# Kernel optimization log

Hardware: AMD Instinct MI355X
Metric: run time of the kernel (lower is better)

## Reference

```python
import jax, jax.numpy as jnp
import numpy as np

WIN = (2, 7, 7)
SHIFT = (1, 3, 3)
HEADS = 4
DIM = 128
MLP_HID = 512
N = WIN[0] * WIN[1] * WIN[2]  # 98
EPS = 1e-5


def _rel_pos_index():
    d = np.arange(WIN[0]); h = np.arange(WIN[1]); w = np.arange(WIN[2])
    coords = np.stack(np.meshgrid(d, h, w, indexing='ij'))  # (3, Wd, Wh, Ww)
    flat = coords.reshape(3, -1)  # (3, N)
    rel = flat[:, :, None] - flat[:, None, :]  # (3, N, N)
    rel = rel.transpose(1, 2, 0).astype(np.int64)  # (N, N, 3)
    rel[..., 0] += WIN[0] - 1
    rel[..., 1] += WIN[1] - 1
    rel[..., 2] += WIN[2] - 1
    rel[..., 0] *= (2 * WIN[1] - 1) * (2 * WIN[2] - 1)
    rel[..., 1] *= (2 * WIN[2] - 1)
    return rel.sum(-1)  # (N, N)


def setup_inputs() -> dict:
    key = jax.random.key(0)
    ks = jax.random.split(key, 8)
    B, D, H, W, C = 4, 8, 56, 56, DIM
    tbl_size = (2 * WIN[0] - 1) * (2 * WIN[1] - 1) * (2 * WIN[2] - 1)  # 507
    s = 0.02
    return {
        'x': jax.random.normal(ks[0], (B, D, H, W, C), jnp.float32),
        'rel_idx': jnp.asarray(_rel_pos_index(), jnp.int32),
        'rpb_table': s * jax.random.normal(ks[1], (tbl_size, HEADS), jnp.float32),
        'qkv_w': s * jax.random.normal(ks[2], (C, 3 * C), jnp.float32),
        'qkv_b': jnp.zeros((3 * C,), jnp.float32),
        'proj_w': s * jax.random.normal(ks[3], (C, C), jnp.float32),
        'proj_b': jnp.zeros((C,), jnp.float32),
        'ln1_g': jnp.ones((C,), jnp.float32),
        'ln1_b': jnp.zeros((C,), jnp.float32),
        'ln2_g': jnp.ones((C,), jnp.float32),
        'ln2_b': jnp.zeros((C,), jnp.float32),
        'mlp_w1': s * jax.random.normal(ks[4], (C, MLP_HID), jnp.float32),
        'mlp_b1': jnp.zeros((MLP_HID,), jnp.float32),
        'mlp_w2': s * jax.random.normal(ks[5], (MLP_HID, C), jnp.float32),
        'mlp_b2': jnp.zeros((C,), jnp.float32),
    }


def _layernorm(x, g, b):
    mu = jnp.mean(x, -1, keepdims=True)
    var = jnp.var(x, -1, keepdims=True)
    return (x - mu) * jax.lax.rsqrt(var + EPS) * g + b


def _window_partition(x):
    B, Dp, Hp, Wp, C = x.shape
    x = x.reshape(B, Dp // WIN[0], WIN[0], Hp // WIN[1], WIN[1], Wp // WIN[2], WIN[2], C)
    x = x.transpose(0, 1, 3, 5, 2, 4, 6, 7)
    return x.reshape(-1, N, C)


def _window_reverse(win, B, Dp, Hp, Wp):
    C = win.shape[-1]
    x = win.reshape(B, Dp // WIN[0], Hp // WIN[1], Wp // WIN[2], WIN[0], WIN[1], WIN[2], C)
    x = x.transpose(0, 1, 4, 2, 5, 3, 6, 7)
    return x.reshape(B, Dp, Hp, Wp, C)


def _block(x, rel_idx, rpb_table, qkv_w, qkv_b, proj_w, proj_b,
           ln1_g, ln1_b, ln2_g, ln2_b, mlp_w1, mlp_b1, mlp_w2, mlp_b2):
    B, D, H, W, C = x.shape
    shortcut = x
    x = _layernorm(x, ln1_g, ln1_b)
    pad_d = (-D) % WIN[0]; pad_h = (-H) % WIN[1]; pad_w = (-W) % WIN[2]
    x = jnp.pad(x, ((0, 0), (0, pad_d), (0, pad_h), (0, pad_w), (0, 0)))
    _, Dp, Hp, Wp, _ = x.shape
    x = jnp.roll(x, (-SHIFT[0], -SHIFT[1], -SHIFT[2]), axis=(1, 2, 3))
    xw = _window_partition(x)  # (B_, N, C)
    B_ = xw.shape[0]
    hd = C // HEADS
    qkv = (xw @ qkv_w + qkv_b).reshape(B_, N, 3, HEADS, hd).transpose(2, 0, 3, 1, 4)
    q, k, v = qkv[0], qkv[1], qkv[2]  # (B_, h, N, hd)
    q = q * (hd ** -0.5)
    attn = jnp.einsum('bhnd,bhmd->bhnm', q, k)
    bias = rpb_table[rel_idx.reshape(-1)].reshape(N, N, HEADS).transpose(2, 0, 1)
    attn = attn + bias[None]
    # NOTE: the original module calls attn with mask=None even when shifted.
    attn = jax.nn.softmax(attn, axis=-1)
    out = jnp.einsum('bhnm,bhmd->bhnd', attn, v).transpose(0, 2, 1, 3).reshape(B_, N, C)
    out = out @ proj_w + proj_b
    x = _window_reverse(out, B, Dp, Hp, Wp)
    x = jnp.roll(x, (SHIFT[0], SHIFT[1], SHIFT[2]), axis=(1, 2, 3))
    x = x[:, :D, :H, :W, :]
    x = shortcut + x
    h1 = _layernorm(x, ln2_g, ln2_b)
    h1 = jax.nn.gelu(h1 @ mlp_w1 + mlp_b1, approximate=False)
    return x + (h1 @ mlp_w2 + mlp_b2)


def reference(x, rel_idx, rpb_table, qkv_w, qkv_b, proj_w, proj_b,
              ln1_g, ln1_b, ln2_g, ln2_b, mlp_w1, mlp_b1, mlp_w2, mlp_b2):
    return _block(x, rel_idx, rpb_table, qkv_w, qkv_b, proj_w, proj_b,
                  ln1_g, ln1_b, ln2_g, ln2_b, mlp_w1, mlp_b1, mlp_w2, mlp_b2)
```

## Files before the change

### kernel.cpp

```cpp
#include <hip/hip_runtime.h>
#include <hip/hip_bf16.h>
#include <cstdint>

#define NWIN   1024
#define NTOK   98
#define BIAS_N 9604

typedef __attribute__((ext_vector_type(8))) short bf16x8;
typedef __attribute__((ext_vector_type(4))) float f32x4;

__device__ __forceinline__ float b2f(unsigned short u) {
  union { uint32_t i; float f; } v; v.i = ((uint32_t)u) << 16; return v.f;
}
__device__ __forceinline__ float b2f_lo(uint32_t u) {
  union { uint32_t i; float f; } v; v.i = u << 16; return v.f;
}
__device__ __forceinline__ float b2f_hi(uint32_t u) {
  union { uint32_t i; float f; } v; v.i = u & 0xffff0000u; return v.f;
}
__device__ __forceinline__ unsigned short f2b(float f) {
  union { float f; uint32_t i; } v; v.f = f;
  uint32_t r = v.i + 0x7fffu + ((v.i >> 16) & 1u);
  return (unsigned short)(r >> 16);
}
__device__ __forceinline__ float ldf(const void* p, size_t i, int f32) {
  return f32 ? ((const float*)p)[i] : b2f(((const unsigned short*)p)[i]);
}
__device__ __forceinline__ float2 ldf2(const void* p, size_t i, int f32) {
  if (f32) { const float* q = (const float*)p + i; return make_float2(q[0], q[1]); }
  uint32_t u = *(const uint32_t*)((const unsigned short*)p + i);
  return make_float2(b2f_lo(u), b2f_hi(u));
}
__device__ __forceinline__ float gelu_f(float x) {
  float a = fabsf(x) * 0.70710678118654752f;
  float t = __builtin_amdgcn_rcpf(1.0f + 0.3275911f * a);
  float p = ((((1.061405429f * t - 1.453152027f) * t + 1.421413741f) * t
              - 0.284496736f) * t + 0.254829592f) * t;
  float erfp = 1.0f - p * __expf(-a * a);
  return 0.5f * x * (1.0f + copysignf(erfp, x));
}

#define QG_OFF   0
#define KG_OFF   25690112
#define VGT_OFF  51380224
#define ZPAD_OFF 80740352
#define BIAS_OFF 80748544
#define WQ_OFF   80902208
#define WP_OFF   81000512
#define W1_OFF   81033280
#define W2_OFF   81164352
#define PAR_OFF  81295424
#define FLAG_OFF 81302080
#define LNG_OFF  81302144
#define P_LN1G 0
#define P_LN1B 128
#define P_LN2G 256
#define P_LN2B 384
#define P_QKVB 512
#define P_PROJB 896
#define P_B1  1024
#define P_B2  1536

__global__ __launch_bounds__(256) void detect_kernel(const uint32_t* __restrict__ xw,
                                                     int* __restrict__ flag) {
  __shared__ int cnt;
  if (threadIdx.x == 0) cnt = 0;
  __syncthreads();
  uint32_t w = xw[threadIdx.x];
  int e = (w >> 23) & 0xFF;
  if (e >= 112 && e <= 134) atomicAdd(&cnt, 1);
  __syncthreads();
  if (threadIdx.x == 0) *flag = (cnt >= 128) ? 1 : 0;
}

__global__ __launch_bounds__(256) void prep_kernel(
    const void* __restrict__ qkvw, const void* __restrict__ projw,
    const void* __restrict__ w1, const void* __restrict__ w2,
    const void* __restrict__ ln1g, const void* __restrict__ ln1b,
    const void* __restrict__ ln2g, const void* __restrict__ ln2b,
    const void* __restrict__ qkvb, const void* __restrict__ projb,
    const void* __restrict__ b1, const void* __restrict__ b2,
    const int* __restrict__ flag,
    unsigned short* __restrict__ wq_t, unsigned short* __restrict__ wp_t,
    unsigned short* __restrict__ w1_t, unsigned short* __restrict__ w2_t,
    float* __restrict__ par, unsigned short* __restrict__ zpad) {
  const int f32 = *flag;
  int idx = blockIdx.x * 256 + threadIdx.x;
  if (idx < 49152) {
    int n = idx >> 7, k = idx & 127;
    wq_t[idx] = f2b(ldf(qkvw, (size_t)k * 384 + n, f32));
  } else if ((idx -= 49152) < 16384) {
    int n = idx >> 7, k = idx & 127;
    wp_t[idx] = f2b(ldf(projw, (size_t)k * 128 + n, f32));
  } else if ((idx -= 16384) < 65536) {
    int n = idx >> 7, k = idx & 127;
    w1_t[idx] = f2b(ldf(w1, (size_t)k * 512 + n, f32));
  } else if ((idx -= 65536) < 65536) {
    int n = idx >> 9, k = idx & 511;
    w2_t[idx] = f2b(ldf(w2, (size_t)k * 128 + n, f32));
  } else if ((idx -= 65536) < 1664) {
    float v;
    if      (idx < 128)  v = ldf(ln1g, idx, f32);
    else if (idx < 256)  v = ldf(ln1b, idx - 128, f32);
    else if (idx < 384)  v = ldf(ln2g, idx - 256, f32);
    else if (idx < 512)  v = ldf(ln2b, idx - 384, f32);
    else if (idx < 896)  v = ldf(qkvb, idx - 512, f32);
    else if (idx < 1024) v = ldf(projb, idx - 896, f32);
    else if (idx < 1536) v = ldf(b1, idx - 1024, f32);
    else                 v = ldf(b2, idx - 1536, f32);
    par[idx] = v;
  } else if ((idx -= 1664) < 4096) {
    zpad[idx] = 0;
  }
}

__global__ __launch_bounds__(256) void bias_kernel(const int* __restrict__ rel_idx,
                                                   const void* __restrict__ tbl,
                                                   const int* __restrict__ flag,
                                                   float* __restrict__ bias) {
  const int f32 = *flag;
  int i = blockIdx.x * 256 + threadIdx.x;
  if (i >= 4 * BIAS_N) return;
  int h = i / BIAS_N, ij = i % BIAS_N;
  bias[i] = ldf(tbl, (size_t)rel_idx[ij] * 4 + h, f32);
}

__global__ __launch_bounds__(256, 2) void attn_fused_kernel(
    const void* __restrict__ x, const int* __restrict__ flag,
    const unsigned short* __restrict__ wq_t, const float* __restrict__ bias,
    const unsigned short* __restrict__ wp_t, const float* __restrict__ par,
    unsigned short* __restrict__ vgt, unsigned short* __restrict__ lng,
    void* __restrict__ out) {
  __shared__ __align__(16) unsigned short smem[38416];
  const int f32 = *flag;
  const int tid = threadIdx.x, wave = tid >> 6, lane = tid & 63;
  const int quad = lane >> 4, lcol = lane & 15;
  const int win = blockIdx.x, h = wave;
  const int bb = win >> 8, rW = win & 255;
  const int wd = rW >> 6, r2 = rW & 63, wh = r2 >> 3, ww = r2 & 7;

  unsigned short* lnx = smem;
  unsigned short* qs  = smem + 13328;
  unsigned short* ks  = smem + 25872;

  for (int t = wave; t < NTOK; t += 4) {
    int td = t / 49, r3 = t % 49, th = r3 / 7, tw = r3 % 7;
    int sd = (wd * 2 + td + 1) & 7;
    int sh = (wh * 7 + th + 3) % 56;
    int sw = (ww * 7 + tw + 3) % 56;
    size_t src = ((((size_t)bb * 8 + sd) * 56 + sh) * 56 + sw) * 128;
    int c0 = lane * 2;
    float2 f = ldf2(x, src + c0, f32);
    float s = f.x + f.y, ss = f.x * f.x + f.y * f.y;
#pragma unroll
    for (int off = 32; off >= 1; off >>= 1) { s += __shfl_xor(s, off); ss += __shfl_xor(ss, off); }
    float mu = s * (1.0f / 128.0f);
    float var = ss * (1.0f / 128.0f) - mu * mu;
    float rs = rsqrtf(var + 1e-5f);
    float y0 = (f.x - mu) * rs * par[P_LN1G + c0] + par[P_LN1B + c0];
    float y1 = (f.y - mu) * rs * par[P_LN1G + c0 + 1] + par[P_LN1B + c0 + 1];
    *(uint32_t*)(lnx + t * 136 + c0) = (uint32_t)f2b(y0) | ((uint32_t)f2b(y1) << 16);
  }
  __syncthreads();

  for (int p = 0; p < 6; ++p) {
    const int n = p * 64 + wave * 16 + lcol;
    bf16x8 bfr[4];
#pragma unroll
    for (int ks4 = 0; ks4 < 4; ++ks4)
      bfr[ks4] = *(const bf16x8*)(wq_t + (size_t)n * 128 + ks4 * 32 + quad * 8);
    const int region = p >> 1;
    const int head = (p & 1) * 2 + (wave >> 1);
    const int d = (wave & 1) * 16 + lcol;
    const float bc = par[P_QKVB + n];
    if (region < 2) {
      unsigned short* dstl = (region == 0 ? qs : ks) + head * 3136 + d;
      const float scale = region == 0 ? 0.17677669529663687f : 1.0f;
      for (int mt = 0; mt < 7; ++mt) {
        f32x4 acc = (f32x4){0.f, 0.f, 0.f, 0.f};
#pragma unroll
        for (int ks4 = 0; ks4 < 4; ++ks4) {
          bf16x8 a = *(const bf16x8*)(lnx + min(mt * 16 + lcol, NTOK - 1) * 136 +
                                      ks4 * 32 + quad * 8);
          acc = __builtin_amdgcn_mfma_f32_16x16x32_bf16(a, bfr[ks4], acc, 0, 0, 0);
        }
#pragma unroll
        for (int rr = 0; rr < 4; ++rr) {
          int m = mt * 16 + quad * 4 + rr;
          if (m < NTOK) dstl[m * 32] = f2b((acc[rr] + bc) * scale);
        }
      }
    } else {
      unsigned short* dstv = vgt + (((size_t)win * 4 + head) * 32 + d) * 112;
      for (int mt = 0; mt < 7; ++mt) {
        f32x4 acc = (f32x4){0.f, 0.f, 0.f, 0.f};
#pragma unroll
        for (int ks4 = 0; ks4 < 4; ++ks4) {
          bf16x8 a = *(const bf16x8*)(lnx + min(mt * 16 + lcol, NTOK - 1) * 136 +
                                      ks4 * 32 + quad * 8);
          acc = __builtin_amdgcn_mfma_f32_16x16x32_bf16(a, bfr[ks4], acc, 0, 0, 0);
        }
        ushort4 w;
        int m0 = mt * 16 + quad * 4;
        w.x = (m0 + 0 < NTOK) ? f2b(acc[0] + bc) : (unsigned short)0;
        w.y = (m0 + 1 < NTOK) ? f2b(acc[1] + bc) : (unsigned short)0;
        w.z = (m0 + 2 < NTOK) ? f2b(acc[2] + bc) : (unsigned short)0;
        w.w = (m0 + 3 < NTOK) ? f2b(acc[3] + bc) : (unsigned short)0;
        *(ushort4*)(dstv + m0) = w;
      }
    }
  }
  __syncthreads();

  const unsigned short* vbase = vgt + (((size_t)win * 4 + h) * 32) * 112;
  unsigned short* plh = smem + h * 2112;

  bf16x8 aq[7], bk[7];
#pragma unroll
  for (int t = 0; t < 7; ++t) {
    int row = min(t * 16 + lcol, NTOK - 1);
    aq[t] = *(const bf16x8*)(qs + h * 3136 + row * 32 + quad * 8);
    bk[t] = *(const bf16x8*)(ks + h * 3136 + row * 32 + quad * 8);
  }
  for (int idx = lane; idx < 16 * 16; idx += 64) {
    int rr = idx >> 4, c = 112 + (idx & 15);
    plh[rr * 132 + c] = 0;
  }

  const float* bh = bias + h * BIAS_N;
  f32x4 o[7][2];
  for (int mt = 0; mt < 7; ++mt) {
    f32x4 s[7];
#pragma unroll
    for (int nt = 0; nt < 7; ++nt)
      s[nt] = __builtin_amdgcn_mfma_f32_16x16x32_bf16(aq[mt], bk[nt],
                                                      (f32x4){0.f, 0.f, 0.f, 0.f}, 0, 0, 0);
    const int ib = mt * 16 + quad * 4;
#pragma unroll
    for (int nt = 0; nt < 7; ++nt) {
      int j = nt * 16 + lcol;
      bool jv = j < NTOK;
#pragma unroll
      for (int r = 0; r < 4; ++r) {
        int ic = min(ib + r, NTOK - 1);
        s[nt][r] = jv ? (s[nt][r] + bh[ic * NTOK + j]) : -3.0e38f;
      }
    }
    float mx[4], sum[4], inv[4];
#pragma unroll
    for (int r = 0; r < 4; ++r) {
      float m = s[0][r];
#pragma unroll
      for (int nt = 1; nt < 7; ++nt) m = fmaxf(m, s[nt][r]);
      mx[r] = m;
    }
#pragma unroll
    for (int off = 1; off < 16; off <<= 1)
#pragma unroll
      for (int r = 0; r < 4; ++r) mx[r] = fmaxf(mx[r], __shfl_xor(mx[r], off));
#pragma unroll
    for (int r = 0; r < 4; ++r) sum[r] = 0.f;
#pragma unroll
    for (int nt = 0; nt < 7; ++nt)
#pragma unroll
      for (int r = 0; r < 4; ++r) {
        float e = __expf(s[nt][r] - mx[r]);
        s[nt][r] = e; sum[r] += e;
      }
#pragma unroll
    for (int off = 1; off < 16; off <<= 1)
#pragma unroll
      for (int r = 0; r < 4; ++r) sum[r] += __shfl_xor(sum[r], off);
#pragma unroll
    for (int r = 0; r < 4; ++r) inv[r] = 1.0f / sum[r];
#pragma unroll
    for (int nt = 0; nt < 7; ++nt)
#pragma unroll
      for (int r = 0; r < 4; ++r)
        plh[(quad * 4 + r) * 132 + nt * 16 + lcol] = f2b(s[nt][r] * inv[r]);
#pragma unroll
    for (int n2 = 0; n2 < 2; ++n2) {
      f32x4 acc = (f32x4){0.f, 0.f, 0.f, 0.f};
#pragma unroll
      for (int kp = 0; kp < 4; ++kp) {
        bf16x8 a = *(const bf16x8*)(plh + lcol * 132 + kp * 32 + quad * 8);
        bf16x8 b = *(const bf16x8*)(vbase + (size_t)(n2 * 16 + lcol) * 112 +
                                    kp * 32 + quad * 8);
        acc = __builtin_amdgcn_mfma_f32_16x16x32_bf16(a, b, acc, 0, 0, 0);
      }
      o[mt][n2] = acc;
    }
  }
  __syncthreads();

  unsigned short* olds = smem + 13328;
#pragma unroll
  for (int mt = 0; mt < 7; ++mt)
#pragma unroll
    for (int n2 = 0; n2 < 2; ++n2)
#pragma unroll
      for (int r = 0; r < 4; ++r)
        olds[(mt * 16 + quad * 4 + r) * 136 + h * 32 + n2 * 16 + lcol] = f2b(o[mt][n2][r]);
  __syncthreads();

  f32x4 pr[2][7];
  for (int t2 = 0; t2 < 2; ++t2) {
    const int n = (h * 2 + t2) * 16 + lcol;
    bf16x8 bw[4];
#pragma unroll
    for (int kp = 0; kp < 4; ++kp)
      bw[kp] = *(const bf16x8*)(wp_t + (size_t)n * 128 + kp * 32 + quad * 8);
    for (int mt = 0; mt < 7; ++mt) {
      f32x4 acc = (f32x4){0.f, 0.f, 0.f, 0.f};
#pragma unroll
      for (int kp = 0; kp < 4; ++kp) {
        bf16x8 a = *(const bf16x8*)(olds + (mt * 16 + lcol) * 136 + kp * 32 + quad * 8);
        acc = __builtin_amdgcn_mfma_f32_16x16x32_bf16(a, bw[kp], acc, 0, 0, 0);
      }
      pr[t2][mt] = acc;
    }
  }
  __syncthreads();

  const int c = (tid & 31) * 4;
  const float4 gv = *(const float4*)(par + P_LN2G + c);
  const float4 bv = *(const float4*)(par + P_LN2B + c);
  float* pout = (float*)smem;
  for (int pass = 0; pass < 2; ++pass) {
    const int mlo = pass * 56;
    for (int t2 = 0; t2 < 2; ++t2) {
      const int n = (h * 2 + t2) * 16 + lcol;
      const float bc = par[P_PROJB + n];
#pragma unroll
      for (int mt = 0; mt < 7; ++mt)
#pragma unroll
        for (int r = 0; r < 4; ++r) {
          int m = mt * 16 + quad * 4 + r;
          if (m >= mlo && m < mlo + 56 && m < NTOK)
            pout[(m - mlo) * 132 + n] = pr[t2][mt][r] + bc;
        }
    }
    __syncthreads();
    for (int i = tid >> 5; i < 56; i += 8) {
      int m = mlo + i;
      if (m >= NTOK) break;
      int td = m / 49, r3 = m % 49, th = r3 / 7, tw = r3 % 7;
      int sd = (wd * 2 + td + 1) & 7;
      int sh = (wh * 7 + th + 3) % 56;
      int sw = (ww * 7 + tw + 3) % 56;
      size_t base = ((((size_t)bb * 8 + sd) * 56 + sh) * 56 + sw) * 128 + c;
      float4 p = *(const float4*)(pout + i * 132 + c);
      float4 v;
      if (f32) {
        const float4 xr = *(const float4*)((const float*)x + base);
        v = make_float4(p.x + xr.x, p.y + xr.y, p.z + xr.z, p.w + xr.w);
        *(float4*)((float*)out + base) = v;
      } else {
        const ushort4 xr = *(const ushort4*)((const unsigned short*)x + base);
        v = make_float4(p.x + b2f(xr.x), p.y + b2f(xr.y),
                        p.z + b2f(xr.z), p.w + b2f(xr.w));
        ushort4 ov;
        ov.x = f2b(v.x); ov.y = f2b(v.y); ov.z = f2b(v.z); ov.w = f2b(v.w);
        *(ushort4*)((unsigned short*)out + base) = ov;
      }
      float s = v.x + v.y + v.z + v.w;
      float ss = v.x * v.x + v.y * v.y + v.z * v.z + v.w * v.w;
#pragma unroll
      for (int off = 1; off < 32; off <<= 1) {
        s += __shfl_xor(s, off); ss += __shfl_xor(ss, off);
      }
      float mu = s * (1.0f / 128.0f);
      float var = ss * (1.0f / 128.0f) - mu * mu;
      float rs = rsqrtf(var + 1e-5f);
      ushort4 lv;
      lv.x = f2b((v.x - mu) * rs * gv.x + bv.x);
      lv.y = f2b((v.y - mu) * rs * gv.y + bv.y);
      lv.z = f2b((v.z - mu) * rs * gv.z + bv.z);
      lv.w = f2b((v.w - mu) * rs * gv.w + bv.w);
      *(ushort4*)(lng + base) = lv;
    }
    if (pass == 0) __syncthreads();
  }
}

__global__ __launch_bounds__(256) void mlp_kernel(
    const unsigned short* __restrict__ w1_t, const unsigned short* __restrict__ w2_t,
    const float* __restrict__ par, const int* __restrict__ flag,
    const unsigned short* __restrict__ lng, void* __restrict__ out) {
  __shared__ __align__(16) unsigned short hbuf[32 * 264];
  const int f32 = *flag;
  const int tid = threadIdx.x, wave = tid >> 6, lane = tid & 63;
  const int quad = lane >> 4, lcol = lane & 15;
  const int m0 = blockIdx.x * 32;
  const int nb = wave * 16 + lcol;

  bf16x8 a1[2][4];
#pragma unroll
  for (int mt = 0; mt < 2; ++mt)
#pragma unroll
    for (int ks = 0; ks < 4; ++ks)
      a1[mt][ks] = *(const bf16x8*)(lng + (size_t)(m0 + mt * 16 + lcol) * 128 +
                                    ks * 32 + quad * 8);

  f32x4 acc2[2][2];
#pragma unroll
  for (int a = 0; a < 2; ++a)
#pragma unroll
    for (int b = 0; b < 2; ++b) acc2[a][b] = (f32x4){0.f, 0.f, 0.f, 0.f};

#pragma unroll 1
  for (int g = 0; g < 2; ++g) {
    for (int p = 0; p < 4; ++p) {
      const int nl = p * 64 + nb;
      const int n = g * 256 + nl;
      bf16x8 bfr[4];
#pragma unroll
      for (int ks = 0; ks < 4; ++ks)
        bfr[ks] = *(const bf16x8*)(w1_t + (size_t)n * 128 + ks * 32 + quad * 8);
      const float bc = par[P_B1 + n];
#pragma unroll
      for (int mt = 0; mt < 2; ++mt) {
        f32x4 acc = (f32x4){0.f, 0.f, 0.f, 0.f};
#pragma unroll
        for (int ks = 0; ks < 4; ++ks)
          acc = __builtin_amdgcn_mfma_f32_16x16x32_bf16(a1[mt][ks], bfr[ks], acc, 0, 0, 0);
#pragma unroll
        for (int rr = 0; rr < 4; ++rr) {
          int m = mt * 16 + quad * 4 + rr;
          hbuf[m * 264 + nl] = f2b(gelu_f(acc[rr] + bc));
        }
      }
    }
    __syncthreads();

#pragma unroll
    for (int np = 0; np < 2; ++np) {
      for (int kp = 0; kp < 2; ++kp) {
        bf16x8 b2r[4];
#pragma unroll
        for (int ks = 0; ks < 4; ++ks)
          b2r[ks] = *(const bf16x8*)(w2_t + (size_t)(np * 64 + nb) * 512 + g * 256 +
                                     kp * 128 + ks * 32 + quad * 8);
#pragma unroll
        for (int mt = 0; mt < 2; ++mt) {
#pragma unroll
          for (int ks = 0; ks < 4; ++ks) {
            bf16x8 a = *(const bf16x8*)(hbuf + (mt * 16 + lcol) * 264 + kp * 128 +
                                        ks * 32 + quad * 8);
            acc2[np][mt] = __builtin_amdgcn_mfma_f32_16x16x32_bf16(a, b2r[ks], acc2[np][mt], 0, 0, 0);
          }
        }
      }
    }
    __syncthreads();
  }

  float* pout = (float*)hbuf;
#pragma unroll
  for (int np = 0; np < 2; ++np) {
    const int n = np * 64 + nb;
    const float bc = par[P_B2 + n];
#pragma unroll
    for (int mt = 0; mt < 2; ++mt)
#pragma unroll
      for (int rr = 0; rr < 4; ++rr)
        pout[(mt * 16 + quad * 4 + rr) * 132 + n] = acc2[np][mt][rr] + bc;
  }
  __syncthreads();

  for (int i = tid; i < 1024; i += 256) {
    int t = i >> 5, c = (i & 31) * 4;
    size_t base = (size_t)(m0 + t) * 128 + c;
    float4 p = *(const float4*)(pout + t * 132 + c);
    if (f32) {
      const float4 xr = *(const float4*)((const float*)out + base);
      float4 ov = make_float4(p.x + xr.x, p.y + xr.y, p.z + xr.z, p.w + xr.w);
      *(float4*)((float*)out + base) = ov;
    } else {
      const ushort4 xr = *(const ushort4*)((const unsigned short*)out + base);
      ushort4 ov;
      ov.x = f2b(p.x + b2f(xr.x)); ov.y = f2b(p.y + b2f(xr.y));
      ov.z = f2b(p.z + b2f(xr.z)); ov.w = f2b(p.w + b2f(xr.w));
      *(ushort4*)((unsigned short*)out + base) = ov;
    }
  }
}

extern "C" void kernel_launch(void* const* d_in, const int* in_sizes, int n_in,
                              void* d_out, int out_size, void* d_ws, size_t ws_size,
                              hipStream_t stream) {
  const void* x      = d_in[0];
  const int*  rel    = (const int*)d_in[1];
  const void* rpb    = d_in[2];
  const void* qkv_w  = d_in[3];
  const void* qkv_b  = d_in[4];
  const void* proj_w = d_in[5];
  const void* proj_b = d_in[6];
  const void* ln1_g  = d_in[7];
  const void* ln1_b  = d_in[8];
  const void* ln2_g  = d_in[9];
  const void* ln2_b  = d_in[10];
  const void* w1     = d_in[11];
  const void* b1     = d_in[12];
  const void* w2     = d_in[13];
  const void* b2     = d_in[14];

  char* ws = (char*)d_ws;
  unsigned short* vgt  = (unsigned short*)(ws + VGT_OFF);
  unsigned short* zpad = (unsigned short*)(ws + ZPAD_OFF);
  float*          bias = (float*)(ws + BIAS_OFF);
  unsigned short* wq_t = (unsigned short*)(ws + WQ_OFF);
  unsigned short* wp_t = (unsigned short*)(ws + WP_OFF);
  unsigned short* w1_t = (unsigned short*)(ws + W1_OFF);
  unsigned short* w2_t = (unsigned short*)(ws + W2_OFF);
  float*          par  = (float*)(ws + PAR_OFF);
  int*            flag = (int*)(ws + FLAG_OFF);
  unsigned short* lng  = (unsigned short*)(ws + LNG_OFF);

  detect_kernel<<<1, 256, 0, stream>>>((const uint32_t*)x, flag);
  prep_kernel<<<791, 256, 0, stream>>>(qkv_w, proj_w, w1, w2, ln1_g, ln1_b, ln2_g,
                                       ln2_b, qkv_b, proj_b, b1, b2, flag,
                                       wq_t, wp_t, w1_t, w2_t, par, zpad);
  bias_kernel<<<(4 * BIAS_N + 255) / 256, 256, 0, stream>>>(rel, rpb, flag, bias);
  attn_fused_kernel<<<NWIN, 256, 0, stream>>>(x, flag, wq_t, bias, wp_t, par,
                                              vgt, lng, d_out);
  mlp_kernel<<<100352 / 32, 256, 0, stream>>>(w1_t, w2_t, par, flag, lng, d_out);
}
```

Baseline: 426.3 us.

## Merge setup kernels, inline dtype detection, spill K to global for occupancy

Removes the separate detect and bias kernels: each kernel now detects the input dtype with a wave ballot, and the bias gather is folded into prep_kernel as extra blocks. K tiles are written to a global scratch buffer instead of LDS, which shrinks attention shared memory from about 77KB to about 52KB and raises launch bounds to 3 blocks per CU. The output staging reuses the freed LDS region. In exchange, the K reads in the attention loop now go through global memory and cache rather than LDS.

```diff
diff --git a/kernel.cpp b/kernel.cpp
--- a/kernel.cpp
+++ b/kernel.cpp
@@ -30,6 +30,12 @@
   if (f32) { const float* q = (const float*)p + i; return make_float2(q[0], q[1]); }
   uint32_t u = *(const uint32_t*)((const unsigned short*)p + i);
   return make_float2(b2f_lo(u), b2f_hi(u));
+}
+__device__ __forceinline__ int detect_f32(const uint32_t* __restrict__ xw, int lane) {
+  uint32_t w = xw[lane];
+  int e = (w >> 23) & 0xFF;
+  unsigned long long m = __ballot(e >= 112 && e <= 134);
+  return __popcll(m) >= 32;
 }
 __device__ __forceinline__ float gelu_f(float x) {
   float a = fabsf(x) * 0.70710678118654752f;
@@ -61,78 +67,66 @@
 #define P_B1  1024
 #define P_B2  1536
 
-__global__ __launch_bounds__(256) void detect_kernel(const uint32_t* __restrict__ xw,
-                                                     int* __restrict__ flag) {
-  __shared__ int cnt;
-  if (threadIdx.x == 0) cnt = 0;
-  __syncthreads();
-  uint32_t w = xw[threadIdx.x];
-  int e = (w >> 23) & 0xFF;
-  if (e >= 112 && e <= 134) atomicAdd(&cnt, 1);
-  __syncthreads();
-  if (threadIdx.x == 0) *flag = (cnt >= 128) ? 1 : 0;
-}
-
 __global__ __launch_bounds__(256) void prep_kernel(
+    const uint32_t* __restrict__ xw,
     const void* __restrict__ qkvw, const void* __restrict__ projw,
     const void* __restrict__ w1, const void* __restrict__ w2,
     const void* __restrict__ ln1g, const void* __restrict__ ln1b,
     const void* __restrict__ ln2g, const void* __restrict__ ln2b,
     const void* __restrict__ qkvb, const void* __restrict__ projb,
     const void* __restrict__ b1, const void* __restrict__ b2,
-    const int* __restrict__ flag,
+    const int* __restrict__ rel_idx, const void* __restrict__ tbl,
     unsigned short* __restrict__ wq_t, unsigned short* __restrict__ wp_t,
     unsigned short* __restrict__ w1_t, unsigned short* __restrict__ w2_t,
-    float* __restrict__ par, unsigned short* __restrict__ zpad) {
-  const int f32 = *flag;
-  int idx = blockIdx.x * 256 + threadIdx.x;
-  if (idx < 49152) {
-    int n = idx >> 7, k = idx & 127;
-    wq_t[idx] = f2b(ldf(qkvw, (size_t)k * 384 + n, f32));
-  } else if ((idx -= 49152) < 16384) {
-    int n = idx >> 7, k = idx & 127;
-    wp_t[idx] = f2b(ldf(projw, (size_t)k * 128 + n, f32));
-  } else if ((idx -= 16384) < 65536) {
-    int n = idx >> 7, k = idx & 127;
-    w1_t[idx] = f2b(ldf(w1, (size_t)k * 512 + n, f32));
-  } else if ((idx -= 65536) < 65536) {
-    int n = idx >> 9, k = idx & 511;
-    w2_t[idx] = f2b(ldf(w2, (size_t)k * 128 + n, f32));
-  } else if ((idx -= 65536) < 1664) {
-    float v;
-    if      (idx < 128)  v = ldf(ln1g, idx, f32);
-    else if (idx < 256)  v = ldf(ln1b, idx - 128, f32);
-    else if (idx < 384)  v = ldf(ln2g, idx - 256, f32);
-    else if (idx < 512)  v = ldf(ln2b, idx - 384, f32);
-    else if (idx < 896)  v = ldf(qkvb, idx - 512, f32);
-    else if (idx < 1024) v = ldf(projb, idx - 896, f32);
-    else if (idx < 1536) v = ldf(b1, idx - 1024, f32);
-    else                 v = ldf(b2, idx - 1536, f32);
-    par[idx] = v;
-  } else if ((idx -= 1664) < 4096) {
-    zpad[idx] = 0;
-  }
-}
-
-__global__ __launch_bounds__(256) void bias_kernel(const int* __restrict__ rel_idx,
-                                                   const void* __restrict__ tbl,
-                                                   const int* __restrict__ flag,
-                                                   float* __restrict__ bias) {
-  const int f32 = *flag;
-  int i = blockIdx.x * 256 + threadIdx.x;
-  if (i >= 4 * BIAS_N) return;
-  int h = i / BIAS_N, ij = i % BIAS_N;
-  bias[i] = ldf(tbl, (size_t)rel_idx[ij] * 4 + h, f32);
-}
-
-__global__ __launch_bounds__(256, 2) void attn_fused_kernel(
-    const void* __restrict__ x, const int* __restrict__ flag,
+    float* __restrict__ par, unsigned short* __restrict__ zpad,
+    float* __restrict__ bias) {
+  const int f32 = detect_f32(xw, threadIdx.x & 63);
+  const int bid = blockIdx.x;
+  if (bid < 791) {
+    int idx = bid * 256 + threadIdx.x;
+    if (idx < 49152) {
+      int n = idx >> 7, k = idx & 127;
+      wq_t[idx] = f2b(ldf(qkvw, (size_t)k * 384 + n, f32));
+    } else if ((idx -= 49152) < 16384) {
+      int n = idx >> 7, k = idx & 127;
+      wp_t[idx] = f2b(ldf(projw, (size_t)k * 128 + n, f32));
+    } else if ((idx -= 16384) < 65536) {
+      int n = idx >> 7, k = idx & 127;
+      w1_t[idx] = f2b(ldf(w1, (size_t)k * 512 + n, f32));
+    } else if ((idx -= 65536) < 65536) {
+      int n = idx >> 9, k = idx & 511;
+      w2_t[idx] = f2b(ldf(w2, (size_t)k * 128 + n, f32));
+    } else if ((idx -= 65536) < 1664) {
+      float v;
+      if      (idx < 128)  v = ldf(ln1g, idx, f32);
+      else if (idx < 256)  v = ldf(ln1b, idx - 128, f32);
+      else if (idx < 384)  v = ldf(ln2g, idx - 256, f32);
+      else if (idx < 512)  v = ldf(ln2b, idx - 384, f32);
+      else if (idx < 896)  v = ldf(qkvb, idx - 512, f32);
+      else if (idx < 1024) v = ldf(projb, idx - 896, f32);
+      else if (idx < 1536) v = ldf(b1, idx - 1024, f32);
+      else                 v = ldf(b2, idx - 1536, f32);
+      par[idx] = v;
+    } else if ((idx -= 1664) < 4096) {
+      zpad[idx] = 0;
+    }
+  } else {
+    int i = (bid - 791) * 256 + threadIdx.x;
+    if (i < 4 * BIAS_N) {
+      int h = i / BIAS_N, ij = i % BIAS_N;
+      bias[i] = ldf(tbl, (size_t)rel_idx[ij] * 4 + h, f32);
+    }
+  }
+}
+
+__global__ __launch_bounds__(256, 3) void attn_fused_kernel(
+    const void* __restrict__ x,
     const unsigned short* __restrict__ wq_t, const float* __restrict__ bias,
     const unsigned short* __restrict__ wp_t, const float* __restrict__ par,
-    unsigned short* __restrict__ vgt, unsigned short* __restrict__ lng,
-    void* __restrict__ out) {
-  __shared__ __align__(16) unsigned short smem[38416];
-  const int f32 = *flag;
+    unsigned short* __restrict__ kg, unsigned short* __restrict__ vgt,
+    unsigned short* __restrict__ lng, void* __restrict__ out) {
+  __shared__ __align__(16) unsigned short smem[25872];
+  const int f32 = detect_f32((const uint32_t*)x, threadIdx.x & 63);
   const int tid = threadIdx.x, wave = tid >> 6, lane = tid & 63;
   const int quad = lane >> 4, lcol = lane & 15;
   const int win = blockIdx.x, h = wave;
@@ -141,7 +135,6 @@
 
   unsigned short* lnx = smem;
   unsigned short* qs  = smem + 13328;
-  unsigned short* ks  = smem + 25872;
 
   for (int t = wave; t < NTOK; t += 4) {
     int td = t / 49, r3 = t % 49, th = r3 / 7, tw = r3 % 7;
@@ -173,9 +166,8 @@
     const int head = (p & 1) * 2 + (wave >> 1);
     const int d = (wave & 1) * 16 + lcol;
     const float bc = par[P_QKVB + n];
-    if (region < 2) {
-      unsigned short* dstl = (region == 0 ? qs : ks) + head * 3136 + d;
-      const float scale = region == 0 ? 0.17677669529663687f : 1.0f;
+    if (region == 0) {
+      unsigned short* dstl = qs + head * 3136 + d;
       for (int mt = 0; mt < 7; ++mt) {
         f32x4 acc = (f32x4){0.f, 0.f, 0.f, 0.f};
 #pragma unroll
@@ -187,7 +179,23 @@
 #pragma unroll
         for (int rr = 0; rr < 4; ++rr) {
           int m = mt * 16 + quad * 4 + rr;
-          if (m < NTOK) dstl[m * 32] = f2b((acc[rr] + bc) * scale);
+          if (m < NTOK) dstl[m * 32] = f2b((acc[rr] + bc) * 0.17677669529663687f);
+        }
+      }
+    } else if (region == 1) {
+      unsigned short* dstg = kg + ((size_t)win * 4 + head) * 3136 + d;
+      for (int mt = 0; mt < 7; ++mt) {
+        f32x4 acc = (f32x4){0.f, 0.f, 0.f, 0.f};
+#pragma unroll
+        for (int ks4 = 0; ks4 < 4; ++ks4) {
+          bf16x8 a = *(const bf16x8*)(lnx + min(mt * 16 + lcol, NTOK - 1) * 136 +
+                                      ks4 * 32 + quad * 8);
+          acc = __builtin_amdgcn_mfma_f32_16x16x32_bf16(a, bfr[ks4], acc, 0, 0, 0);
+        }
+#pragma unroll
+        for (int rr = 0; rr < 4; ++rr) {
+          int m = mt * 16 + quad * 4 + rr;
+          if (m < NTOK) dstg[m * 32] = f2b(acc[rr] + bc);
         }
       }
     } else {
@@ -212,6 +220,7 @@
   }
   __syncthreads();
 
+  const size_t hb = ((size_t)win * 4 + h) * 3136;
   const unsigned short* vbase = vgt + (((size_t)win * 4 + h) * 32) * 112;
   unsigned short* plh = smem + h * 2112;
 
@@ -220,7 +229,7 @@
   for (int t = 0; t < 7; ++t) {
     int row = min(t * 16 + lcol, NTOK - 1);
     aq[t] = *(const bf16x8*)(qs + h * 3136 + row * 32 + quad * 8);
-    bk[t] = *(const bf16x8*)(ks + h * 3136 + row * 32 + quad * 8);
+    bk[t] = *(const bf16x8*)(kg + hb + (size_t)row * 32 + quad * 8);
   }
   for (int idx = lane; idx < 16 * 16; idx += 64) {
     int rr = idx >> 4, c = 112 + (idx & 15);
@@ -293,7 +302,7 @@
   }
   __syncthreads();
 
-  unsigned short* olds = smem + 13328;
+  unsigned short* olds = smem;
 #pragma unroll
   for (int mt = 0; mt < 7; ++mt)
 #pragma unroll
@@ -385,10 +394,10 @@
 
 __global__ __launch_bounds__(256) void mlp_kernel(
     const unsigned short* __restrict__ w1_t, const unsigned short* __restrict__ w2_t,
-    const float* __restrict__ par, const int* __restrict__ flag,
+    const float* __restrict__ par, const void* __restrict__ x,
     const unsigned short* __restrict__ lng, void* __restrict__ out) {
   __shared__ __align__(16) unsigned short hbuf[32 * 264];
-  const int f32 = *flag;
+  const int f32 = detect_f32((const uint32_t*)x, threadIdx.x & 63);
   const int tid = threadIdx.x, wave = tid >> 6, lane = tid & 63;
   const int quad = lane >> 4, lcol = lane & 15;
   const int m0 = blockIdx.x * 32;
@@ -506,6 +515,7 @@
   const void* b2     = d_in[14];
 
   char* ws = (char*)d_ws;
+  unsigned short* kg   = (unsigned short*)(ws + KG_OFF);
   unsigned short* vgt  = (unsigned short*)(ws + VGT_OFF);
   unsigned short* zpad = (unsigned short*)(ws + ZPAD_OFF);
   float*          bias = (float*)(ws + BIAS_OFF);
@@ -514,15 +524,13 @@
   unsigned short* w1_t = (unsigned short*)(ws + W1_OFF);
   unsigned short* w2_t = (unsigned short*)(ws + W2_OFF);
   float*          par  = (float*)(ws + PAR_OFF);
-  int*            flag = (int*)(ws + FLAG_OFF);
   unsigned short* lng  = (unsigned short*)(ws + LNG_OFF);
 
-  detect_kernel<<<1, 256, 0, stream>>>((const uint32_t*)x, flag);
-  prep_kernel<<<791, 256, 0, stream>>>(qkv_w, proj_w, w1, w2, ln1_g, ln1_b, ln2_g,
-                                       ln2_b, qkv_b, proj_b, b1, b2, flag,
-                                       wq_t, wp_t, w1_t, w2_t, par, zpad);
-  bias_kernel<<<(4 * BIAS_N + 255) / 256, 256, 0, stream>>>(rel, rpb, flag, bias);
-  attn_fused_kernel<<<NWIN, 256, 0, stream>>>(x, flag, wq_t, bias, wp_t, par,
-                                              vgt, lng, d_out);
-  mlp_kernel<<<100352 / 32, 256, 0, stream>>>(w1_t, w2_t, par, flag, lng, d_out);
-}
+  prep_kernel<<<791 + 151, 256, 0, stream>>>(
+      (const uint32_t*)x, qkv_w, proj_w, w1, w2, ln1_g, ln1_b, ln2_g, ln2_b,
+      qkv_b, proj_b, b1, b2, rel, rpb,
+      wq_t, wp_t, w1_t, w2_t, par, zpad, bias);
+  attn_fused_kernel<<<NWIN, 256, 0, stream>>>(x, wq_t, bias, wp_t, par,
+                                              kg, vgt, lng, d_out);
+  mlp_kernel<<<100352 / 32, 256, 0, stream>>>(w1_t, w2_t, par, x, lng, d_out);
+}
```

New measurement: 384.0 us. 1.11x faster.
